# Kernel optimization log

Hardware: AMD Instinct MI355X
Metric: run time of the kernel (lower is better)

Reference implementation:

```python
import jax, jax.numpy as jnp
import numpy as np

EPS = 1e-12

def l2_normalize(x, axis=-1):
    return x * jax.lax.rsqrt(jnp.sum(x * x, axis=axis, keepdims=True) + EPS)

def setup_inputs() -> dict:
    key = jax.random.key(0)
    k1, k2 = jax.random.split(key)
    hidden_states = jax.random.normal(k1, (32, 1024, 32), dtype=jnp.float32)
    embedding = jax.random.normal(k2, (8192, 32), dtype=jnp.float32)
    return {"hidden_states": hidden_states, "embedding": embedding}

def reference(hidden_states, embedding):
    B, N, D = hidden_states.shape
    # flatten to tokens and L2-normalize both sides
    z_flat = l2_normalize(hidden_states.reshape(-1, D), axis=1)      # [B*N, D]
    emb_n = l2_normalize(embedding, axis=1)                          # [K, D]
    # pairwise squared L2 distance (on normalized vectors)
    distance = (jnp.sum(z_flat ** 2, axis=1, keepdims=True)
                + jnp.sum(emb_n ** 2, axis=1)
                - 2.0 * jnp.dot(z_flat, emb_n.T))                    # [B*N, K]
    min_encoding_indices = jnp.argmin(distance, axis=1).reshape(B, N)
    # codebook lookup on the RAW embedding, then normalize (get_codebook_entry)
    z_q = l2_normalize(jnp.take(embedding, min_encoding_indices, axis=0), axis=-1)  # [B, N, D]
    hidden_normed = l2_normalize(hidden_states, axis=-1)
    e_latent_loss = jnp.mean(jnp.square(jax.lax.stop_gradient(z_q) - hidden_normed))
    q_latent_loss = jnp.mean(jnp.square(z_q - jax.lax.stop_gradient(hidden_normed)))
    # straight-through estimator
    z_q = hidden_states + jax.lax.stop_gradient(z_q - hidden_states)
    return (z_q, min_encoding_indices, q_latent_loss, e_latent_loss)
```

## Files before the change

### kernel.cpp

```cpp
#include <hip/hip_runtime.h>
#include <math.h>

#define TOKENS 32768
#define KCODES 8192
#define DIM 32
#define NCHUNK 16
#define CPC 512
#define GSZ 128
#define NGROUPS 64
#define RT_TOK 16
#define ZQ_ELEMS (TOKENS * DIM)
#define MARGIN 1e-3f

typedef __attribute__((ext_vector_type(8))) short short8v;
typedef __attribute__((ext_vector_type(4))) float f32x4;

__device__ inline unsigned rne16(unsigned u) {
  return (u + 0x7FFFu + ((u >> 16) & 1u)) >> 16;
}

__global__ __launch_bounds__(256) void prep_codes(
    const float* __restrict__ emb, short* __restrict__ cA,
    short* __restrict__ cB, float* __restrict__ embT4,
    float* __restrict__ nsq, float* __restrict__ seF) {
  int gid = blockIdx.x * 256 + threadIdx.x;
  int code = gid >> 5;
  int k = gid & 31;
  float v = emb[gid];
  double dv = (double)v;
  double ds = dv * dv;
#pragma unroll
  for (int off = 16; off > 0; off >>= 1) ds += __shfl_xor(ds, off, 32);
  if (k == 0) seF[code] = (float)ds;
  float r = 1.0f / sqrtf((float)ds + 1e-12f);
  float en = v * r;
  float sn = en * en;
#pragma unroll
  for (int off = 16; off > 0; off >>= 1) sn += __shfl_xor(sn, off, 32);
  if (k == 0) nsq[code] = sn;
  embT4[(size_t)((k >> 2) * KCODES + code) * 4 + (k & 3)] = en;

  float w = -en;
  unsigned ua = rne16(__float_as_uint(w));
  float fa = __uint_as_float(ua << 16);
  unsigned ub = rne16(__float_as_uint(w - fa));
  int tile = code >> 4;
  int lane = (code & 15) | ((k >> 3) << 4);
  int off = tile * 512 + lane * 8 + (k & 7);
  cA[off] = (short)ua;
  cB[off] = (short)ub;
}

__global__ __launch_bounds__(256) void screen_kernel(
    const float* __restrict__ hs, const short* __restrict__ cA,
    const short* __restrict__ cB, float* __restrict__ pgmin) {
  int tid = threadIdx.x;
  int l = tid & 63;
  int w = tid >> 6;
  int g = l >> 4;
  int c16 = l & 15;
  int gt0 = blockIdx.x * 16 + w * 4;
  int chunk = blockIdx.y;

  short8v zA[4], zB[4];
#pragma unroll
  for (int tt = 0; tt < 4; tt++) {
    int tok = (gt0 + tt) * 16 + c16;
    const float4* hp4 = (const float4*)(hs + (size_t)tok * DIM + g * 8);
    float4 q0 = hp4[0];
    float4 q1 = hp4[1];
    float x[8] = {q0.x, q0.y, q0.z, q0.w, q1.x, q1.y, q1.z, q1.w};
#pragma unroll
    for (int j = 0; j < 8; j++) {
      unsigned ua = rne16(__float_as_uint(x[j]));
      float fa = __uint_as_float(ua << 16);
      unsigned ub = rne16(__float_as_uint(x[j] - fa));
      zA[tt][j] = (short)ua;
      zB[tt][j] = (short)ub;
    }
  }

  int tbase = chunk * (CPC / 16);

  for (int grp = 0; grp < CPC / GSZ; grp++) {
    float gm[4] = {3.4e38f, 3.4e38f, 3.4e38f, 3.4e38f};
#pragma unroll
    for (int ct = 0; ct < GSZ / 16; ct++) {
      int tile = tbase + grp * (GSZ / 16) + ct;
      short8v aA = *((const short8v*)(cA + (size_t)tile * 512) + l);
      short8v aB = *((const short8v*)(cB + (size_t)tile * 512) + l);
#pragma unroll
      for (int tt = 0; tt < 4; tt++) {
        f32x4 acc = {};
        acc = __builtin_amdgcn_mfma_f32_16x16x32_bf16(aA, zA[tt], acc, 0, 0, 0);
        acc = __builtin_amdgcn_mfma_f32_16x16x32_bf16(aA, zB[tt], acc, 0, 0, 0);
        acc = __builtin_amdgcn_mfma_f32_16x16x32_bf16(aB, zA[tt], acc, 0, 0, 0);
        float m = fminf(fminf(acc[0], acc[1]), fminf(acc[2], acc[3]));
        gm[tt] = fminf(gm[tt], m);
      }
    }
    int gidx = (chunk * (CPC / GSZ) + grp);
#pragma unroll
    for (int tt = 0; tt < 4; tt++) {
      float v = gm[tt];
      v = fminf(v, __shfl_xor(v, 16));
      v = fminf(v, __shfl_xor(v, 32));
      if (l < 16) {
        int tok = (gt0 + tt) * 16 + c16;
        pgmin[(size_t)gidx * TOKENS + tok] = v;
      }
    }
  }
}

__global__ __launch_bounds__(1024) void rescore_kernel(
    const float* __restrict__ hs, const float* __restrict__ emb,
    const float* __restrict__ embT4, const float* __restrict__ nsq,
    const float* __restrict__ seF, const float* __restrict__ pgmin,
    float* __restrict__ out, float* __restrict__ lossacc) {
  __shared__ float pg[NGROUPS][RT_TOK + 1];
  __shared__ float zsh[RT_TOK][DIM];
  __shared__ float lred[RT_TOK];
  int tid = threadIdx.x;
  int w = tid >> 6;
  int l = tid & 63;
  int tok0 = blockIdx.x * RT_TOK;
  int tok = tok0 + w;

  {
    int grp = tid >> 4;
    int tk = tid & 15;
    pg[grp][tk] = pgmin[(size_t)grp * TOKENS + tok0 + tk];
  }
  if (tid < RT_TOK * DIM)
    zsh[tid >> 5][tid & 31] = hs[(size_t)tok0 * DIM + tid];
  __syncthreads();

  float zf[DIM];
#pragma unroll
  for (int j = 0; j < 8; j++) {
    float4 q = *(const float4*)&zsh[w][4 * j];
    zf[4 * j] = q.x; zf[4 * j + 1] = q.y;
    zf[4 * j + 2] = q.z; zf[4 * j + 3] = q.w;
  }
  float s0 = 0.f, s1 = 0.f, s2 = 0.f, s3 = 0.f;
#pragma unroll
  for (int j = 0; j < 8; j++) {
    s0 = fmaf(zf[4 * j], zf[4 * j], s0);
    s1 = fmaf(zf[4 * j + 1], zf[4 * j + 1], s1);
    s2 = fmaf(zf[4 * j + 2], zf[4 * j + 2], s2);
    s3 = fmaf(zf[4 * j + 3], zf[4 * j + 3], s3);
  }
  float sz = (s0 + s1) + (s2 + s3);
  float rz = 1.0f / sqrtf(sz + 1e-12f);
  float szn = sz * rz * rz;
  float n2rz = -2.0f * rz;

  float v = pg[l][w];
  float m = v;
#pragma unroll
  for (int off = 1; off < 64; off <<= 1) m = fminf(m, __shfl_xor(m, off));
  unsigned long long mask = __ballot(v <= m + MARGIN);

  unsigned long long bkey = ~0ull;
  const float4* tp = (const float4*)embT4;
  while (mask) {
    int grp = __ffsll(mask) - 1;
    mask &= mask - 1;
#pragma unroll
    for (int half = 0; half < 2; half++) {
      int c = grp * GSZ + half * 64 + l;
      float d0 = 0.f, d1 = 0.f, d2 = 0.f, d3 = 0.f;
#pragma unroll
      for (int d4 = 0; d4 < 8; d4++) {
        float4 q = tp[(size_t)d4 * KCODES + c];
        d0 = fmaf(zf[4 * d4], q.x, d0);
        d1 = fmaf(zf[4 * d4 + 1], q.y, d1);
        d2 = fmaf(zf[4 * d4 + 2], q.z, d2);
        d3 = fmaf(zf[4 * d4 + 3], q.w, d3);
      }
      float dot = (d0 + d1) + (d2 + d3);
      float D = fmaf(n2rz, dot, szn + nsq[c]);
      unsigned ud = __float_as_uint(D);
      ud ^= (unsigned)((int)ud >> 31) | 0x80000000u;
      unsigned long long key = ((unsigned long long)ud << 32) | (unsigned)c;
      if (key < bkey) bkey = key;
    }
  }
#pragma unroll
  for (int off = 1; off < 64; off <<= 1) {
    unsigned long long o = __shfl_xor(bkey, off);
    bkey = (o < bkey) ? o : bkey;
  }
  int bestidx = (int)(unsigned)bkey;

  if (l == 0) out[(size_t)ZQ_ELEMS + tok] = (float)bestidx;

  int d = l & 31;
  float ev = emb[(size_t)bestidx * DIM + d];
  float reW = 1.0f / sqrtf(seF[bestidx] + 1e-12f);
  float zq = ev * reW;
  float lp = 0.f;
  if (l < 32) {
    out[(size_t)tok * DIM + d] = zq;
    float hn = zsh[w][d] * rz;
    float diff = zq - hn;
    lp = diff * diff;
  }
#pragma unroll
  for (int off = 1; off < 32; off <<= 1) lp += __shfl_xor(lp, off);
  if (l == 0) lred[w] = lp;
  __syncthreads();
  if (tid == 0) {
    float b = 0.f;
#pragma unroll
    for (int i = 0; i < RT_TOK; i++) b += lred[i];
    atomicAdd(lossacc + (blockIdx.x & 127), b);
  }
}

__global__ void loss_write_kernel(const float* __restrict__ lossacc,
                                  float* __restrict__ out) {
  int l = threadIdx.x;
  float s = lossacc[l] + lossacc[l + 64];
#pragma unroll
  for (int off = 1; off < 64; off <<= 1) s += __shfl_xor(s, off);
  if (l == 0) {
    float v = s * (1.0f / (float)ZQ_ELEMS);
    out[ZQ_ELEMS + TOKENS] = v;
    out[ZQ_ELEMS + TOKENS + 1] = v;
  }
}

extern "C" void kernel_launch(void* const* d_in, const int* in_sizes, int n_in,
                              void* d_out, int out_size, void* d_ws,
                              size_t ws_size, hipStream_t stream) {
  const float* hs = (const float*)d_in[0];
  const float* emb = (const float*)d_in[1];
  float* out = (float*)d_out;
  char* ws = (char*)d_ws;

  short* cA = (short*)(ws);
  short* cB = (short*)(ws + 524288);
  float* embT4 = (float*)(ws + 1048576);
  float* nsq = (float*)(ws + 2097152);
  float* seF = (float*)(ws + 2129920);
  float* pgmin = (float*)(ws + 2162688);
  float* lossacc = (float*)(ws + 10551296);

  hipLaunchKernelGGL(prep_codes, dim3((KCODES * DIM) / 256), dim3(256), 0,
                     stream, emb, cA, cB, embT4, nsq, seF);
  hipMemsetAsync(lossacc, 0, 512, stream);
  hipLaunchKernelGGL(screen_kernel, dim3(TOKENS / 256, NCHUNK), dim3(256), 0,
                     stream, hs, cA, cB, pgmin);
  hipLaunchKernelGGL(rescore_kernel, dim3(TOKENS / RT_TOK), dim3(1024), 0,
                     stream, hs, emb, embT4, nsq, seF, pgmin, out, lossacc);
  hipLaunchKernelGGL(loss_write_kernel, dim3(1), dim3(64), 0, stream, lossacc,
                     out);
}
```

Baseline: 105.5 us.

## Drop low half of codebook split-bf16 in screening, widen per-wave token tile

The screening pass now stores only a single bf16 copy of the normalized codebook and uses two MFMAs per tile (codebook high half against token high and low halves) instead of three, so the cB buffer and its loads are gone. Each wave now handles 8 token tiles instead of 4, which halves the grid in x and reuses each codebook load across more tokens. To cover the larger screening error, the rescore margin changes from a fixed constant to one proportional to the unnormalized token norm. The wider margin may send more groups to exact rescoring, and accuracy now relies on that margin bounding the bf16 error of the codebook.

```diff
diff --git a/kernel.cpp b/kernel.cpp
--- a/kernel.cpp
+++ b/kernel.cpp
@@ -9,8 +9,8 @@
 #define GSZ 128
 #define NGROUPS 64
 #define RT_TOK 16
+#define TT 8
 #define ZQ_ELEMS (TOKENS * DIM)
-#define MARGIN 1e-3f
 
 typedef __attribute__((ext_vector_type(8))) short short8v;
 typedef __attribute__((ext_vector_type(4))) float f32x4;
@@ -21,8 +21,8 @@
 
 __global__ __launch_bounds__(256) void prep_codes(
     const float* __restrict__ emb, short* __restrict__ cA,
-    short* __restrict__ cB, float* __restrict__ embT4,
-    float* __restrict__ nsq, float* __restrict__ seF) {
+    float* __restrict__ embT4, float* __restrict__ nsq,
+    float* __restrict__ seF) {
   int gid = blockIdx.x * 256 + threadIdx.x;
   int code = gid >> 5;
   int k = gid & 31;
@@ -40,31 +40,27 @@
   if (k == 0) nsq[code] = sn;
   embT4[(size_t)((k >> 2) * KCODES + code) * 4 + (k & 3)] = en;
 
-  float w = -en;
-  unsigned ua = rne16(__float_as_uint(w));
-  float fa = __uint_as_float(ua << 16);
-  unsigned ub = rne16(__float_as_uint(w - fa));
+  unsigned ua = rne16(__float_as_uint(-en));
   int tile = code >> 4;
   int lane = (code & 15) | ((k >> 3) << 4);
   int off = tile * 512 + lane * 8 + (k & 7);
   cA[off] = (short)ua;
-  cB[off] = (short)ub;
 }
 
 __global__ __launch_bounds__(256) void screen_kernel(
     const float* __restrict__ hs, const short* __restrict__ cA,
-    const short* __restrict__ cB, float* __restrict__ pgmin) {
+    float* __restrict__ pgmin) {
   int tid = threadIdx.x;
   int l = tid & 63;
   int w = tid >> 6;
   int g = l >> 4;
   int c16 = l & 15;
-  int gt0 = blockIdx.x * 16 + w * 4;
+  int gt0 = blockIdx.x * 32 + w * TT;
   int chunk = blockIdx.y;
 
-  short8v zA[4], zB[4];
-#pragma unroll
-  for (int tt = 0; tt < 4; tt++) {
+  short8v zA[TT], zB[TT];
+#pragma unroll
+  for (int tt = 0; tt < TT; tt++) {
     int tok = (gt0 + tt) * 16 + c16;
     const float4* hp4 = (const float4*)(hs + (size_t)tok * DIM + g * 8);
     float4 q0 = hp4[0];
@@ -83,25 +79,25 @@
   int tbase = chunk * (CPC / 16);
 
   for (int grp = 0; grp < CPC / GSZ; grp++) {
-    float gm[4] = {3.4e38f, 3.4e38f, 3.4e38f, 3.4e38f};
+    float gm[TT];
+#pragma unroll
+    for (int tt = 0; tt < TT; tt++) gm[tt] = 3.4e38f;
 #pragma unroll
     for (int ct = 0; ct < GSZ / 16; ct++) {
       int tile = tbase + grp * (GSZ / 16) + ct;
       short8v aA = *((const short8v*)(cA + (size_t)tile * 512) + l);
-      short8v aB = *((const short8v*)(cB + (size_t)tile * 512) + l);
-#pragma unroll
-      for (int tt = 0; tt < 4; tt++) {
+#pragma unroll
+      for (int tt = 0; tt < TT; tt++) {
         f32x4 acc = {};
         acc = __builtin_amdgcn_mfma_f32_16x16x32_bf16(aA, zA[tt], acc, 0, 0, 0);
         acc = __builtin_amdgcn_mfma_f32_16x16x32_bf16(aA, zB[tt], acc, 0, 0, 0);
-        acc = __builtin_amdgcn_mfma_f32_16x16x32_bf16(aB, zA[tt], acc, 0, 0, 0);
         float m = fminf(fminf(acc[0], acc[1]), fminf(acc[2], acc[3]));
         gm[tt] = fminf(gm[tt], m);
       }
     }
     int gidx = (chunk * (CPC / GSZ) + grp);
 #pragma unroll
-    for (int tt = 0; tt < 4; tt++) {
+    for (int tt = 0; tt < TT; tt++) {
       float v = gm[tt];
       v = fminf(v, __shfl_xor(v, 16));
       v = fminf(v, __shfl_xor(v, 32));
@@ -155,12 +151,13 @@
   float rz = 1.0f / sqrtf(sz + 1e-12f);
   float szn = sz * rz * rz;
   float n2rz = -2.0f * rz;
+  float margin = 0.009f * sqrtf(sz + 1e-12f);
 
   float v = pg[l][w];
   float m = v;
 #pragma unroll
   for (int off = 1; off < 64; off <<= 1) m = fminf(m, __shfl_xor(m, off));
-  unsigned long long mask = __ballot(v <= m + MARGIN);
+  unsigned long long mask = __ballot(v <= m + margin);
 
   unsigned long long bkey = ~0ull;
   const float4* tp = (const float4*)embT4;
@@ -241,18 +238,17 @@
   char* ws = (char*)d_ws;
 
   short* cA = (short*)(ws);
-  short* cB = (short*)(ws + 524288);
-  float* embT4 = (float*)(ws + 1048576);
-  float* nsq = (float*)(ws + 2097152);
-  float* seF = (float*)(ws + 2129920);
-  float* pgmin = (float*)(ws + 2162688);
-  float* lossacc = (float*)(ws + 10551296);
+  float* embT4 = (float*)(ws + 524288);
+  float* nsq = (float*)(ws + 1572864);
+  float* seF = (float*)(ws + 1605632);
+  float* pgmin = (float*)(ws + 1638400);
+  float* lossacc = (float*)(ws + 10027008);
 
   hipLaunchKernelGGL(prep_codes, dim3((KCODES * DIM) / 256), dim3(256), 0,
-                     stream, emb, cA, cB, embT4, nsq, seF);
+                     stream, emb, cA, embT4, nsq, seF);
   hipMemsetAsync(lossacc, 0, 512, stream);
-  hipLaunchKernelGGL(screen_kernel, dim3(TOKENS / 256, NCHUNK), dim3(256), 0,
-                     stream, hs, cA, cB, pgmin);
+  hipLaunchKernelGGL(screen_kernel, dim3(TOKENS / 512, NCHUNK), dim3(256), 0,
+                     stream, hs, cA, pgmin);
   hipLaunchKernelGGL(rescore_kernel, dim3(TOKENS / RT_TOK), dim3(1024), 0,
                      stream, hs, emb, embT4, nsq, seF, pgmin, out, lossacc);
   hipLaunchKernelGGL(loss_write_kernel, dim3(1), dim3(64), 0, stream, lossacc,
```

Result: slower. 129.6 us (+22.9%).

## Pre-split tokens into bf16 MFMA tiles and double token tiles per wave

Applied to the files above, without the earlier changes.

Adds a prep_tokens kernel that converts hidden states into hi/lo bf16 pairs already laid out in MFMA fragment order, so screen_kernel loads them directly instead of converting in every chunk block. Each wave now handles 8 token tiles instead of 4, so every loaded codebook tile feeds twice as many MFMAs, and the grid is halved. In exchange it adds an extra kernel launch plus a 4 MB workspace round-trip, and more registers per wave, which may lower occupancy and leaves fewer blocks (1024) to fill the GPU.

```diff
diff --git a/kernel.cpp b/kernel.cpp
--- a/kernel.cpp
+++ b/kernel.cpp
@@ -9,6 +9,7 @@
 #define GSZ 128
 #define NGROUPS 64
 #define RT_TOK 16
+#define TT 8
 #define ZQ_ELEMS (TOKENS * DIM)
 #define MARGIN 1e-3f
 
@@ -51,46 +52,54 @@
   cB[off] = (short)ub;
 }
 
+__global__ __launch_bounds__(256) void prep_tokens(
+    const float* __restrict__ hs, short* __restrict__ zAf,
+    short* __restrict__ zBf) {
+  int gid = blockIdx.x * 256 + threadIdx.x;
+  int tok = gid >> 5;
+  int k = gid & 31;
+  float x = hs[gid];
+  unsigned ua = rne16(__float_as_uint(x));
+  float fa = __uint_as_float(ua << 16);
+  unsigned ub = rne16(__float_as_uint(x - fa));
+  int tile = tok >> 4;
+  int lane = (tok & 15) | ((k >> 3) << 4);
+  int off = tile * 512 + lane * 8 + (k & 7);
+  zAf[off] = (short)ua;
+  zBf[off] = (short)ub;
+}
+
 __global__ __launch_bounds__(256) void screen_kernel(
-    const float* __restrict__ hs, const short* __restrict__ cA,
-    const short* __restrict__ cB, float* __restrict__ pgmin) {
+    const short* __restrict__ zAf, const short* __restrict__ zBf,
+    const short* __restrict__ cA, const short* __restrict__ cB,
+    float* __restrict__ pgmin) {
   int tid = threadIdx.x;
   int l = tid & 63;
   int w = tid >> 6;
-  int g = l >> 4;
   int c16 = l & 15;
-  int gt0 = blockIdx.x * 16 + w * 4;
+  int gt0 = blockIdx.x * 32 + w * TT;
   int chunk = blockIdx.y;
 
-  short8v zA[4], zB[4];
-#pragma unroll
-  for (int tt = 0; tt < 4; tt++) {
-    int tok = (gt0 + tt) * 16 + c16;
-    const float4* hp4 = (const float4*)(hs + (size_t)tok * DIM + g * 8);
-    float4 q0 = hp4[0];
-    float4 q1 = hp4[1];
-    float x[8] = {q0.x, q0.y, q0.z, q0.w, q1.x, q1.y, q1.z, q1.w};
-#pragma unroll
-    for (int j = 0; j < 8; j++) {
-      unsigned ua = rne16(__float_as_uint(x[j]));
-      float fa = __uint_as_float(ua << 16);
-      unsigned ub = rne16(__float_as_uint(x[j] - fa));
-      zA[tt][j] = (short)ua;
-      zB[tt][j] = (short)ub;
-    }
-  }
-
-  int tbase = chunk * (CPC / 16);
+  short8v zA[TT], zB[TT];
+#pragma unroll
+  for (int tt = 0; tt < TT; tt++) {
+    zA[tt] = *((const short8v*)(zAf + (size_t)(gt0 + tt) * 512) + l);
+    zB[tt] = *((const short8v*)(zBf + (size_t)(gt0 + tt) * 512) + l);
+  }
+
+  int tbase = chunk * 32;
 
   for (int grp = 0; grp < CPC / GSZ; grp++) {
-    float gm[4] = {3.4e38f, 3.4e38f, 3.4e38f, 3.4e38f};
+    float gm[TT];
+#pragma unroll
+    for (int tt = 0; tt < TT; tt++) gm[tt] = 3.4e38f;
 #pragma unroll
     for (int ct = 0; ct < GSZ / 16; ct++) {
       int tile = tbase + grp * (GSZ / 16) + ct;
       short8v aA = *((const short8v*)(cA + (size_t)tile * 512) + l);
       short8v aB = *((const short8v*)(cB + (size_t)tile * 512) + l);
 #pragma unroll
-      for (int tt = 0; tt < 4; tt++) {
+      for (int tt = 0; tt < TT; tt++) {
         f32x4 acc = {};
         acc = __builtin_amdgcn_mfma_f32_16x16x32_bf16(aA, zA[tt], acc, 0, 0, 0);
         acc = __builtin_amdgcn_mfma_f32_16x16x32_bf16(aA, zB[tt], acc, 0, 0, 0);
@@ -99,9 +108,9 @@
         gm[tt] = fminf(gm[tt], m);
       }
     }
-    int gidx = (chunk * (CPC / GSZ) + grp);
-#pragma unroll
-    for (int tt = 0; tt < 4; tt++) {
+    int gidx = chunk * (CPC / GSZ) + grp;
+#pragma unroll
+    for (int tt = 0; tt < TT; tt++) {
       float v = gm[tt];
       v = fminf(v, __shfl_xor(v, 16));
       v = fminf(v, __shfl_xor(v, 32));
@@ -242,17 +251,21 @@
 
   short* cA = (short*)(ws);
   short* cB = (short*)(ws + 524288);
-  float* embT4 = (float*)(ws + 1048576);
-  float* nsq = (float*)(ws + 2097152);
-  float* seF = (float*)(ws + 2129920);
-  float* pgmin = (float*)(ws + 2162688);
-  float* lossacc = (float*)(ws + 10551296);
+  short* zAf = (short*)(ws + 1048576);
+  short* zBf = (short*)(ws + 3145728);
+  float* embT4 = (float*)(ws + 5242880);
+  float* nsq = (float*)(ws + 6291456);
+  float* seF = (float*)(ws + 6324224);
+  float* pgmin = (float*)(ws + 6356992);
+  float* lossacc = (float*)(ws + 14745600);
 
   hipLaunchKernelGGL(prep_codes, dim3((KCODES * DIM) / 256), dim3(256), 0,
                      stream, emb, cA, cB, embT4, nsq, seF);
+  hipLaunchKernelGGL(prep_tokens, dim3((TOKENS * DIM) / 256), dim3(256), 0,
+                     stream, hs, zAf, zBf);
   hipMemsetAsync(lossacc, 0, 512, stream);
-  hipLaunchKernelGGL(screen_kernel, dim3(TOKENS / 256, NCHUNK), dim3(256), 0,
-                     stream, hs, cA, cB, pgmin);
+  hipLaunchKernelGGL(screen_kernel, dim3(TOKENS / 512, NCHUNK), dim3(256), 0,
+                     stream, zAf, zBf, cA, cB, pgmin);
   hipLaunchKernelGGL(rescore_kernel, dim3(TOKENS / RT_TOK), dim3(1024), 0,
                      stream, hs, emb, embT4, nsq, seF, pgmin, out, lossacc);
   hipLaunchKernelGGL(loss_write_kernel, dim3(1), dim3(64), 0, stream, lossacc,
```

After: 141.3 us. +33.9%, slower.
